# Optimization experiments

Hardware: AMD Instinct MI355X
Metric: run time of the kernel (lower is better)

Reference implementation:

```python
import jax, jax.numpy as jnp
import numpy as np

PI2 = 6.283185307


def setup_inputs() -> dict:
    key = jax.random.key(0)
    k1, k2, k3, k4 = jax.random.split(key, 4)
    T, n_mix, n_dim = 262144, 64, 16
    data = jax.random.normal(k1, (T, n_dim), dtype=jnp.float32)
    # mixture weights: positive, roughly summing to 1
    wghts = jax.random.uniform(k2, (n_mix, 1), dtype=jnp.float32, minval=0.5, maxval=1.5) / n_mix
    means = jax.random.normal(k3, (n_mix, n_dim), dtype=jnp.float32)
    # diagonal covariances: strictly positive
    dcovs = jax.random.uniform(k4, (n_mix, n_dim), dtype=jnp.float32, minval=0.5, maxval=1.5)
    return {"data": data, "wghts": wghts, "means": means, "dcovs": dcovs}


def reference(data, wghts, means, dcovs):
    # data: (T, D); wghts: (M, 1); means: (M, D); dcovs: (M, D)
    n_dim = data.shape[1]
    c = 1.0 / np.sqrt(PI2 ** n_dim)  # Gaussian normalizer (2*pi)^{-D/2}
    c_dets = 1.0 / jnp.sqrt(jnp.prod(dcovs, axis=1))  # (M,) |Sigma|^{-1/2}
    dprecs = 1.0 / dcovs  # (M, D) diagonal precisions
    diff = data[:, None, :] - means[None, :, :]  # (T, M, D)
    mhbs_dist = jnp.einsum('tmd,md->tm', diff * diff, dprecs)  # (T, M)
    probs = (wghts[:, 0] * c * c_dets)[None, :] * jnp.exp(-0.5 * mhbs_dist)  # (T, M)
    likes = jnp.sum(probs, axis=1)  # (T,)
    log_likes = jnp.mean(jnp.log(likes))
    posteriors = probs / likes[:, None]  # (T, M)
    e_means = posteriors @ means  # (T, D) weighted mean of component means
    return (log_likes, e_means)
```

## Files before the change

kernel.cpp:

```cpp
#include <hip/hip_runtime.h>

#define T_TOTAL 262144
#define NMIX 64
#define NDIM 16

typedef short bf16x8 __attribute__((ext_vector_type(8)));
typedef unsigned short u16x8 __attribute__((ext_vector_type(8)));
typedef float f32x4 __attribute__((ext_vector_type(4)));

__device__ __forceinline__ unsigned short f2bf(float f) {
    union { float f; unsigned u; } v; v.f = f;
    unsigned r = v.u + 0x7fff + ((v.u >> 16) & 1);
    return (unsigned short)(r >> 16);
}
__device__ __forceinline__ float bf2f(unsigned short s) {
    union { unsigned u; float f; } v; v.u = ((unsigned)s) << 16;
    return v.f;
}

#define L_WH   0
#define L_WL   5120
#define L_MUT  10240
#define L_A2   12544
#define L_RED  12800
#define L_F    12864
#define L_P    33344

__global__ __launch_bounds__(256, 3) void gmm_main(const float* __restrict__ data,
                                                   const float* __restrict__ wghts,
                                                   const float* __restrict__ means,
                                                   const float* __restrict__ dcovs,
                                                   float* __restrict__ out,
                                                   float* __restrict__ part) {
    __shared__ __align__(16) char lds[42560];
    const int tid  = threadIdx.x;
    const int w    = tid >> 6;
    const int lane = tid & 63;
    const int gi   = lane & 15;
    const int gq   = lane >> 4;
    const size_t tblk = (size_t)blockIdx.x * 128;

    const int row = tid >> 1, half = tid & 1;
    const float4* xp = (const float4*)(data + (tblk + row) * 16 + half * 8);
    float4 xa = xp[0], xb = xp[1];

    if (tid < 64) {
        const int m = tid;
        const float LOG2E = 1.4426950408889634f;
        const float LOG2_2PI = 2.6514961294723187f;
        float dc[16], mu[16];
        {
            const float4* dp = (const float4*)(dcovs + m * 16);
            const float4* mp = (const float4*)(means + m * 16);
#pragma unroll
            for (int q = 0; q < 4; ++q) {
                float4 d4 = dp[q], m4 = mp[q];
                dc[q*4+0]=d4.x; dc[q*4+1]=d4.y; dc[q*4+2]=d4.z; dc[q*4+3]=d4.w;
                mu[q*4+0]=m4.x; mu[q*4+1]=m4.y; mu[q*4+2]=m4.z; mu[q*4+3]=m4.w;
            }
        }
        u16x8 ghv[2], glv[2], hhv[2], hlv[2];
        float sumlog = 0.0f, qsum = 0.0f;
        unsigned short* mut = (unsigned short*)(lds + L_MUT);
#pragma unroll
        for (int d = 0; d < 16; ++d) {
            float pr = 1.0f / dc[d];
            float g = -0.5f * LOG2E * pr;
            float h = LOG2E * pr * mu[d];
            unsigned short gh = f2bf(g), hh = f2bf(h);
            ghv[d >> 3][d & 7] = gh;   glv[d >> 3][d & 7] = f2bf(g - bf2f(gh));
            hhv[d >> 3][d & 7] = hh;   hlv[d >> 3][d & 7] = f2bf(h - bf2f(hh));
            mut[d * 72 + m] = f2bf(mu[d]);
            sumlog += __builtin_amdgcn_logf(dc[d]);
            qsum   += pr * mu[d] * mu[d];
        }
        char* wrh = lds + L_WH + m * 80;
        char* wrl = lds + L_WL + m * 80;
        *(u16x8*)(wrh)      = ghv[0];  *(u16x8*)(wrh + 16) = ghv[1];
        *(u16x8*)(wrh + 32) = hhv[0];  *(u16x8*)(wrh + 48) = hhv[1];
        *(u16x8*)(wrl)      = glv[0];  *(u16x8*)(wrl + 16) = glv[1];
        *(u16x8*)(wrl + 32) = hlv[0];  *(u16x8*)(wrl + 48) = hlv[1];
        float log2C = __builtin_amdgcn_logf(wghts[m]) - 8.0f * LOG2_2PI - 0.5f * sumlog;
        ((float*)(lds + L_A2))[m] = log2C - 0.5f * LOG2E * qsum;
    }

    {
        int fw = row >> 5, lr = row & 31;
        float xv[8] = {xa.x, xa.y, xa.z, xa.w, xb.x, xb.y, xb.z, xb.w};
        u16x8 vh2, vl2, vhx, vlx;
#pragma unroll
        for (int d = 0; d < 8; ++d) {
            float q = xv[d] * xv[d];
            unsigned short qh = f2bf(q);
            vh2[d] = qh;               vl2[d] = f2bf(q - bf2f(qh));
            unsigned short xh = f2bf(xv[d]);
            vhx[d] = xh;               vlx[d] = f2bf(xv[d] - bf2f(xh));
        }
        char* fb = lds + L_F + fw * 5120 + lr * 80;
        *(u16x8*)(fb + half * 16)        = vh2;
        *(u16x8*)(fb + 32 + half * 16)   = vhx;
        char* fl = fb + 2560;
        *(u16x8*)(fl + half * 16)        = vl2;
        *(u16x8*)(fl + 32 + half * 16)   = vlx;
    }
    __syncthreads();

    bf16x8 bh[4], bl[4];
    float a2v[4];
#pragma unroll
    for (int c = 0; c < 4; ++c) {
        bh[c] = *(const bf16x8*)(lds + L_WH + (c * 16 + gi) * 80 + gq * 16);
        bl[c] = *(const bf16x8*)(lds + L_WL + (c * 16 + gi) * 80 + gq * 16);
        a2v[c] = ((const float*)(lds + L_A2))[c * 16 + gi];
    }
    bf16x8 mf0 = *(const bf16x8*)(lds + L_MUT + gi * 144 + gq * 16);
    bf16x8 mf1 = *(const bf16x8*)(lds + L_MUT + gi * 144 + 64 + gq * 16);

    const char* fbase = lds + L_F + w * 5120;
    char* pbase = lds + L_P + w * 2304;
    float ll_acc = 0.0f;

#pragma unroll
    for (int rt = 0; rt < 2; ++rt) {
        bf16x8 ah = *(const bf16x8*)(fbase + (rt * 16 + gi) * 80 + gq * 16);
        bf16x8 al = *(const bf16x8*)(fbase + 2560 + (rt * 16 + gi) * 80 + gq * 16);

        f32x4 pacc[4];
#pragma unroll
        for (int c = 0; c < 4; ++c) {
            f32x4 a = {0.0f, 0.0f, 0.0f, 0.0f};
            a = __builtin_amdgcn_mfma_f32_16x16x32_bf16(al, bh[c], a, 0, 0, 0);
            a = __builtin_amdgcn_mfma_f32_16x16x32_bf16(ah, bl[c], a, 0, 0, 0);
            a = __builtin_amdgcn_mfma_f32_16x16x32_bf16(ah, bh[c], a, 0, 0, 0);
            pacc[c] = a;
        }

        float p[4][4], prow[4], inv[4];
#pragma unroll
        for (int reg = 0; reg < 4; ++reg) {
#pragma unroll
            for (int c = 0; c < 4; ++c)
                p[c][reg] = __builtin_amdgcn_exp2f(pacc[c][reg] + a2v[c]);
            prow[reg] = (p[0][reg] + p[1][reg]) + (p[2][reg] + p[3][reg]);
        }
#pragma unroll
        for (int reg = 0; reg < 4; ++reg) {
            float v = prow[reg];
            v += __shfl_xor(v, 1);  v += __shfl_xor(v, 2);
            v += __shfl_xor(v, 4);  v += __shfl_xor(v, 8);
            v = fmaxf(v, 1e-35f);
            ll_acc += __builtin_amdgcn_logf(v);
            inv[reg] = __builtin_amdgcn_rcpf(v);
        }

#pragma unroll
        for (int c = 0; c < 4; ++c)
#pragma unroll
            for (int reg = 0; reg < 4; ++reg)
                *(unsigned short*)(pbase + (gq * 4 + reg) * 144 + (c * 16 + gi) * 2) =
                    f2bf(p[c][reg]);

        bf16x8 ap0 = *(const bf16x8*)(pbase + gi * 144 + gq * 16);
        bf16x8 ap1 = *(const bf16x8*)(pbase + gi * 144 + 64 + gq * 16);
        f32x4 e = {0.0f, 0.0f, 0.0f, 0.0f};
        e = __builtin_amdgcn_mfma_f32_16x16x32_bf16(ap0, mf0, e, 0, 0, 0);
        e = __builtin_amdgcn_mfma_f32_16x16x32_bf16(ap1, mf1, e, 0, 0, 0);

        size_t trow = tblk + (size_t)w * 32 + rt * 16 + gq * 4;
#pragma unroll
        for (int reg = 0; reg < 4; ++reg)
            out[1 + (trow + reg) * 16 + gi] = e[reg] * inv[reg];
    }

    ll_acc += __shfl_xor(ll_acc, 16);
    ll_acc += __shfl_xor(ll_acc, 32);
    if (lane == 0) ((float*)(lds + L_RED))[w] = ll_acc;
    __syncthreads();
    if (tid == 0) {
        float* r = (float*)(lds + L_RED);
        part[blockIdx.x] = (r[0] + r[1]) + (r[2] + r[3]);
    }
}

__global__ void gmm_fin(const float* __restrict__ part, float* __restrict__ out) {
    __shared__ double red[4];
    const int tid = threadIdx.x;
    double s = 0.0;
#pragma unroll
    for (int k = 0; k < 8; ++k) s += (double)part[tid + k * 256];
#pragma unroll
    for (int off = 32; off > 0; off >>= 1) s += __shfl_down(s, off, 64);
    const int wv = tid >> 6, lane = tid & 63;
    if (lane == 0) red[wv] = s;
    __syncthreads();
    if (tid == 0) {
        const double LN2 = 0.6931471805599453;
        double tot = (red[0] + red[1]) + (red[2] + red[3]);
        out[0] = (float)(tot * LN2 / (double)T_TOTAL);
    }
}

extern "C" void kernel_launch(void* const* d_in, const int* in_sizes, int n_in,
                              void* d_out, int out_size, void* d_ws, size_t ws_size,
                              hipStream_t stream) {
    const float* data  = (const float*)d_in[0];
    const float* wghts = (const float*)d_in[1];
    const float* means = (const float*)d_in[2];
    const float* dcovs = (const float*)d_in[3];
    float* out  = (float*)d_out;
    float* part = (float*)d_ws;

    gmm_main<<<T_TOTAL / 128, 256, 0, stream>>>(data, wghts, means, dcovs, out, part);
    gmm_fin<<<1, 256, 0, stream>>>(part, out);
}
```

Measured before the change: 88.04 us.

## Fuse final reduction via last-block atomic counter and parallelize per-component setup

Drops the separate finalize kernel. Each block publishes its partial log-likelihood and increments a global atomic counter, and the last block to arrive sums all partials in double precision. The per-block parameter precompute now spreads each mixture component over four threads instead of one, shortening the serial prologue before the first barrier. This adds a memset launch, release/acquire atomics, and an extra barrier in every block.

```diff
diff --git a/kernel.cpp b/kernel.cpp
--- a/kernel.cpp
+++ b/kernel.cpp
@@ -1,11 +1,13 @@
 #include <hip/hip_runtime.h>
 
 #define T_TOTAL 262144
+#define NBLOCKS 2048
 #define NMIX 64
 #define NDIM 16
 
 typedef short bf16x8 __attribute__((ext_vector_type(8)));
 typedef unsigned short u16x8 __attribute__((ext_vector_type(8)));
+typedef unsigned short u16x4 __attribute__((ext_vector_type(4)));
 typedef float f32x4 __attribute__((ext_vector_type(4)));
 
 __device__ __forceinline__ unsigned short f2bf(float f) {
@@ -23,6 +25,8 @@
 #define L_MUT  10240
 #define L_A2   12544
 #define L_RED  12800
+#define L_FLAG 12816
+#define L_DRED 12824
 #define L_F    12864
 #define L_P    33344
 
@@ -31,7 +35,8 @@
                                                    const float* __restrict__ means,
                                                    const float* __restrict__ dcovs,
                                                    float* __restrict__ out,
-                                                   float* __restrict__ part) {
+                                                   float* __restrict__ part,
+                                                   unsigned* __restrict__ cnt) {
     __shared__ __align__(16) char lds[42560];
     const int tid  = threadIdx.x;
     const int w    = tid >> 6;
@@ -44,44 +49,43 @@
     const float4* xp = (const float4*)(data + (tblk + row) * 16 + half * 8);
     float4 xa = xp[0], xb = xp[1];
 
-    if (tid < 64) {
-        const int m = tid;
+    {
+        const int m  = tid >> 2;
+        const int ql = tid & 3;
         const float LOG2E = 1.4426950408889634f;
         const float LOG2_2PI = 2.6514961294723187f;
-        float dc[16], mu[16];
-        {
-            const float4* dp = (const float4*)(dcovs + m * 16);
-            const float4* mp = (const float4*)(means + m * 16);
-#pragma unroll
-            for (int q = 0; q < 4; ++q) {
-                float4 d4 = dp[q], m4 = mp[q];
-                dc[q*4+0]=d4.x; dc[q*4+1]=d4.y; dc[q*4+2]=d4.z; dc[q*4+3]=d4.w;
-                mu[q*4+0]=m4.x; mu[q*4+1]=m4.y; mu[q*4+2]=m4.z; mu[q*4+3]=m4.w;
-            }
-        }
-        u16x8 ghv[2], glv[2], hhv[2], hlv[2];
+        const float4 d4 = *(const float4*)(dcovs + m * 16 + ql * 4);
+        const float4 m4 = *(const float4*)(means + m * 16 + ql * 4);
+        const float wm = wghts[m];
+        float dc[4] = {d4.x, d4.y, d4.z, d4.w};
+        float mu[4] = {m4.x, m4.y, m4.z, m4.w};
+        u16x4 ghv, glv, hhv, hlv;
         float sumlog = 0.0f, qsum = 0.0f;
         unsigned short* mut = (unsigned short*)(lds + L_MUT);
 #pragma unroll
-        for (int d = 0; d < 16; ++d) {
-            float pr = 1.0f / dc[d];
+        for (int j = 0; j < 4; ++j) {
+            float pr = __builtin_amdgcn_rcpf(dc[j]);
             float g = -0.5f * LOG2E * pr;
-            float h = LOG2E * pr * mu[d];
-            unsigned short gh = f2bf(g), hh = f2bf(h);
-            ghv[d >> 3][d & 7] = gh;   glv[d >> 3][d & 7] = f2bf(g - bf2f(gh));
-            hhv[d >> 3][d & 7] = hh;   hlv[d >> 3][d & 7] = f2bf(h - bf2f(hh));
-            mut[d * 72 + m] = f2bf(mu[d]);
-            sumlog += __builtin_amdgcn_logf(dc[d]);
-            qsum   += pr * mu[d] * mu[d];
+            float h = LOG2E * pr * mu[j];
+            unsigned short gH = f2bf(g), hH = f2bf(h);
+            ghv[j] = gH;  glv[j] = f2bf(g - bf2f(gH));
+            hhv[j] = hH;  hlv[j] = f2bf(h - bf2f(hH));
+            mut[(ql * 4 + j) * 72 + m] = f2bf(mu[j]);
+            sumlog += __builtin_amdgcn_logf(dc[j]);
+            qsum   += pr * mu[j] * mu[j];
         }
         char* wrh = lds + L_WH + m * 80;
         char* wrl = lds + L_WL + m * 80;
-        *(u16x8*)(wrh)      = ghv[0];  *(u16x8*)(wrh + 16) = ghv[1];
-        *(u16x8*)(wrh + 32) = hhv[0];  *(u16x8*)(wrh + 48) = hhv[1];
-        *(u16x8*)(wrl)      = glv[0];  *(u16x8*)(wrl + 16) = glv[1];
-        *(u16x8*)(wrl + 32) = hlv[0];  *(u16x8*)(wrl + 48) = hlv[1];
-        float log2C = __builtin_amdgcn_logf(wghts[m]) - 8.0f * LOG2_2PI - 0.5f * sumlog;
-        ((float*)(lds + L_A2))[m] = log2C - 0.5f * LOG2E * qsum;
+        *(u16x4*)(wrh + ql * 8)      = ghv;
+        *(u16x4*)(wrh + 32 + ql * 8) = hhv;
+        *(u16x4*)(wrl + ql * 8)      = glv;
+        *(u16x4*)(wrl + 32 + ql * 8) = hlv;
+        sumlog += __shfl_xor(sumlog, 1); sumlog += __shfl_xor(sumlog, 2);
+        qsum   += __shfl_xor(qsum, 1);   qsum   += __shfl_xor(qsum, 2);
+        if (ql == 0) {
+            float log2C = __builtin_amdgcn_logf(wm) - 8.0f * LOG2_2PI - 0.5f * sumlog;
+            ((float*)(lds + L_A2))[m] = log2C - 0.5f * LOG2E * qsum;
+        }
     }
 
     {
@@ -178,25 +182,27 @@
     __syncthreads();
     if (tid == 0) {
         float* r = (float*)(lds + L_RED);
-        part[blockIdx.x] = (r[0] + r[1]) + (r[2] + r[3]);
-    }
-}
-
-__global__ void gmm_fin(const float* __restrict__ part, float* __restrict__ out) {
-    __shared__ double red[4];
-    const int tid = threadIdx.x;
-    double s = 0.0;
-#pragma unroll
-    for (int k = 0; k < 8; ++k) s += (double)part[tid + k * 256];
-#pragma unroll
-    for (int off = 32; off > 0; off >>= 1) s += __shfl_down(s, off, 64);
-    const int wv = tid >> 6, lane = tid & 63;
-    if (lane == 0) red[wv] = s;
+        float pv = (r[0] + r[1]) + (r[2] + r[3]);
+        __hip_atomic_store(&part[blockIdx.x], pv, __ATOMIC_RELEASE, __HIP_MEMORY_SCOPE_AGENT);
+        unsigned old = __hip_atomic_fetch_add(cnt, 1u, __ATOMIC_ACQ_REL, __HIP_MEMORY_SCOPE_AGENT);
+        *(int*)(lds + L_FLAG) = (old == NBLOCKS - 1) ? 1 : 0;
+    }
     __syncthreads();
-    if (tid == 0) {
-        const double LN2 = 0.6931471805599453;
-        double tot = (red[0] + red[1]) + (red[2] + red[3]);
-        out[0] = (float)(tot * LN2 / (double)T_TOTAL);
+    if (*(int*)(lds + L_FLAG)) {
+        double s = 0.0;
+#pragma unroll
+        for (int k = 0; k < 8; ++k)
+            s += (double)__hip_atomic_load(&part[tid + k * 256], __ATOMIC_ACQUIRE,
+                                           __HIP_MEMORY_SCOPE_AGENT);
+#pragma unroll
+        for (int off = 32; off > 0; off >>= 1) s += __shfl_down(s, off, 64);
+        if (lane == 0) ((double*)(lds + L_DRED))[w] = s;
+        __syncthreads();
+        if (tid == 0) {
+            double* dr = (double*)(lds + L_DRED);
+            const double LN2 = 0.6931471805599453;
+            out[0] = (float)(((dr[0] + dr[1]) + (dr[2] + dr[3])) * LN2 / (double)T_TOTAL);
+        }
     }
 }
 
@@ -209,7 +215,8 @@
     const float* dcovs = (const float*)d_in[3];
     float* out  = (float*)d_out;
     float* part = (float*)d_ws;
-
-    gmm_main<<<T_TOTAL / 128, 256, 0, stream>>>(data, wghts, means, dcovs, out, part);
-    gmm_fin<<<1, 256, 0, stream>>>(part, out);
-}
+    unsigned* cnt = (unsigned*)((char*)d_ws + 8192);
+
+    hipMemsetAsync(cnt, 0, 4, stream);
+    gmm_main<<<NBLOCKS, 256, 0, stream>>>(data, wghts, means, dcovs, out, part, cnt);
+}
```

Result: slower. 189.7 us (+115.5%).
